# Kernel optimization log

Hardware: AMD Instinct MI355X
Metric: run time of the kernel (lower is better)

Reference implementation:

```python
import jax, jax.numpy as jnp
import numpy as np

N_NODES = 4096
D_FEAT = 256


def _interp_linear_2x(x):
    # Matches F.interpolate(mode='linear', scale_factor=2, align_corners=False)
    # applied along the node axis. x: [N, D] -> [2N, D]
    n = x.shape[0]
    out_i = jnp.arange(2 * n, dtype=jnp.float32)
    src = jnp.clip((out_i + 0.5) * 0.5 - 0.5, 0.0, float(n - 1))
    i0 = jnp.floor(src).astype(jnp.int32)
    i1 = jnp.minimum(i0 + 1, n - 1)
    w = (src - i0.astype(jnp.float32))[:, None]
    return x[i0] * (1.0 - w) + x[i1] * w


def _nearest_neighbor_idx(x):
    # argmin over pairwise Euclidean distances with diagonal excluded.
    # Squared distances give the same argmin as torch.cdist.
    sq = jnp.sum(x * x, axis=1)
    d2 = sq[:, None] + sq[None, :] - 2.0 * (x @ x.T)  # [2N, 2N]
    m = x.shape[0]
    d2 = jnp.where(jnp.eye(m, dtype=bool), jnp.inf, d2)
    return jnp.argmin(d2, axis=1)


def setup_inputs() -> dict:
    key = jax.random.key(0)
    k1, k2, k3, k4 = jax.random.split(key, 4)
    x = jax.random.normal(k1, (N_NODES, D_FEAT), dtype=jnp.float32)
    adj = jax.random.uniform(k2, (N_NODES, N_NODES), dtype=jnp.float32)
    # Xavier-uniform-ish init for the two GCN weights
    lim = float(np.sqrt(6.0 / (D_FEAT + D_FEAT)))
    W1 = jax.random.uniform(k3, (D_FEAT, D_FEAT), jnp.float32, -lim, lim)
    W2 = jax.random.uniform(k4, (D_FEAT, D_FEAT), jnp.float32, -lim, lim)
    return {"x": x, "adj": adj, "W1": W1, "W2": W2}


def reference(x, adj, W1, W2):
    # conv1: adj @ (x @ W1)
    h = adj @ (x @ W1)                      # [N, D]
    x2 = _interp_linear_2x(h)               # [2N, D]
    # nearest-neighbor one-hot adjacency, then conv2.
    # one_hot(nn_idx) @ support == support[nn_idx] (exact same math)
    nn_idx = _nearest_neighbor_idx(x2)      # [2N]
    support = x2 @ W2                       # [2N, D]
    return support[nn_idx]                  # [2N, D]
```

## Files before the change

### kernel.cpp

```cpp
#include <hip/hip_runtime.h>
#include <hip/hip_bf16.h>
#include <cstdint>

typedef __attribute__((ext_vector_type(8))) __bf16 bf16x8;
typedef __attribute__((ext_vector_type(4))) float f32x4;

static __device__ __forceinline__ unsigned short f2bf(float f) {
  return __builtin_bit_cast(unsigned short, (__bf16)f);
}
static __device__ __forceinline__ unsigned pack2(float a, float b) {
  return (unsigned)f2bf(a) | ((unsigned)f2bf(b) << 16);
}
#define GLDS(src, dst) __builtin_amdgcn_global_load_lds( \
    (const __attribute__((address_space(1))) void*)(src), \
    (__attribute__((address_space(3))) void*)(dst), 16, 0, 0)


__global__ void transpose_w_kernel(const float* __restrict__ W1, const float* __restrict__ W2,
                                   unsigned short* __restrict__ W1t, unsigned short* __restrict__ W2t) {
  int i = blockIdx.x * 256 + threadIdx.x;
  int k = i >> 8, n = i & 255;
  W1t[n * 256 + k] = f2bf(W1[k * 256 + n]);
  W2t[n * 256 + k] = f2bf(W2[k * 256 + n]);
}

__global__ void upsample_kernel(const unsigned short* __restrict__ hs,
                                unsigned short* __restrict__ x2b, float* __restrict__ sq) {
  int row = blockIdx.x * 4 + (threadIdx.x >> 6);
  int c = (threadIdx.x & 63) * 4;
  float s = (row + 0.5f) * 0.5f - 0.5f;
  s = fminf(fmaxf(s, 0.0f), 4095.0f);
  float fl = floorf(s);
  int i0 = (int)fl;
  int i1 = min((int)fl + 1, 4095);
  float w = s - fl;
  float v0[4] = {0.f, 0.f, 0.f, 0.f}, v1[4] = {0.f, 0.f, 0.f, 0.f};
  #pragma unroll
  for (int k = 0; k < 8; ++k) {
    ushort4 u0 = *(const ushort4*)&hs[(size_t)k * 4096 * 256 + i0 * 256 + c];
    ushort4 u1 = *(const ushort4*)&hs[(size_t)k * 4096 * 256 + i1 * 256 + c];
    v0[0] += __builtin_bit_cast(float, (unsigned)u0.x << 16);
    v0[1] += __builtin_bit_cast(float, (unsigned)u0.y << 16);
    v0[2] += __builtin_bit_cast(float, (unsigned)u0.z << 16);
    v0[3] += __builtin_bit_cast(float, (unsigned)u0.w << 16);
    v1[0] += __builtin_bit_cast(float, (unsigned)u1.x << 16);
    v1[1] += __builtin_bit_cast(float, (unsigned)u1.y << 16);
    v1[2] += __builtin_bit_cast(float, (unsigned)u1.z << 16);
    v1[3] += __builtin_bit_cast(float, (unsigned)u1.w << 16);
  }
  float p = 0.f;
  ushort4 st;
  unsigned short* sp = (unsigned short*)&st;
  #pragma unroll
  for (int e = 0; e < 4; ++e) {
    float v = v0[e] * (1.0f - w) + v1[e] * w;
    sp[e] = f2bf(v);
    p += v * v;
  }
  *(ushort4*)&x2b[(size_t)row * 256 + c] = st;
  #pragma unroll
  for (int m = 32; m > 0; m >>= 1) p += __shfl_down(p, m, 64);
  if ((threadIdx.x & 63) == 0) sq[row] = p;
}

__global__ void argmin_reduce_kernel(const unsigned* __restrict__ pv,
                                     unsigned* __restrict__ pck) {
  int row = blockIdx.x * 256 + threadIdx.x;
  int cr = row >> 7;
  unsigned best = 0xFFFFFFFFu;
  for (int c = 0; c <= cr; ++c) best = min(best, pv[(size_t)c * 8192 + row]);
  for (int c = cr + 1; c < 64; ++c) best = min(best, pv[(size_t)(64 + c) * 8192 + row]);
  pck[row] = best & 0x1FFFu;
}

__global__ void gather_kernel(const float* __restrict__ support,
                              const unsigned* __restrict__ pck,
                              float* __restrict__ out) {
  int gid = blockIdx.x * 256 + threadIdx.x;
  int row = gid >> 6;
  int c4 = (gid & 63) * 4;
  unsigned idx = pck[row];
  *(float4*)&out[(size_t)row * 256 + c4] = *(const float4*)&support[(size_t)idx * 256 + c4];
}

__launch_bounds__(256, 3)
__global__ void gram_kernel(const unsigned short* __restrict__ X,
                            const float* __restrict__ sq,
                            unsigned* __restrict__ pv) {
  __shared__ alignas(16) unsigned short As[128 * 64];
  __shared__ alignas(16) unsigned short Bs[128 * 64];
  __shared__ unsigned mrgr[2][128];
  __shared__ unsigned mrgc[2][128];

  const int tid = threadIdx.x;
  const int wid = tid >> 6;
  const int lane = tid & 63;
  const int g = lane >> 4, lr = lane & 15;
  const int wr = wid >> 1, wc = wid & 1;

  int t = blockIdx.x;
  int bi = (int)((sqrtf(8.0f * (float)t + 1.0f) - 1.0f) * 0.5f);
  while ((bi + 1) * (bi + 2) / 2 <= t) ++bi;
  while (bi * (bi + 1) / 2 > t) --bi;
  const int bx = bi;
  const int by = t - bi * (bi + 1) / 2;
  const int m0 = bx * 128;
  const int n0 = by * 128;
  const bool diag = (bx == by);

  const int srow = tid >> 3;
  const int ssc = (tid & 7) ^ (srow & 7);
  const unsigned short* aBase = X + (size_t)(m0 + srow) * 256 + ssc * 8;
  const unsigned short* bBase = X + (size_t)(n0 + srow) * 256 + ssc * 8;
  unsigned short* const aDst = As + (size_t)(tid >> 6) * 512;
  unsigned short* const bDst = Bs + (size_t)(tid >> 6) * 512;

  f32x4 acc[4][4];
  const f32x4 fzero = {0.f, 0.f, 0.f, 0.f};
  #pragma unroll
  for (int i = 0; i < 4; ++i)
    #pragma unroll
    for (int j = 0; j < 4; ++j) acc[i][j] = fzero;

  #pragma unroll
  for (int ks = 0; ks < 4; ++ks) {
    #pragma unroll
    for (int it = 0; it < 4; ++it)
      GLDS(aBase + it * 8192 + ks * 64, aDst + it * 2048);
    #pragma unroll
    for (int it = 0; it < 4; ++it)
      GLDS(bBase + it * 8192 + ks * 64, bDst + it * 2048);
    __syncthreads();
    #pragma unroll
    for (int kk = 0; kk < 2; ++kk) {
      const int ch = (kk * 4 + g) ^ (lr & 7);
      bf16x8 b[4];
      #pragma unroll
      for (int j = 0; j < 4; ++j)
        b[j] = *(const bf16x8*)&Bs[(wc * 64 + j * 16 + lr) * 64 + ch * 8];
      #pragma unroll
      for (int i = 0; i < 4; ++i) {
        bf16x8 a = *(const bf16x8*)&As[(wr * 64 + i * 16 + lr) * 64 + ch * 8];
        #pragma unroll
        for (int j = 0; j < 4; ++j)
          acc[i][j] = __builtin_amdgcn_mfma_f32_16x16x32_bf16(a, b[j], acc[i][j], 0, 0, 0);
      }
    }
    __syncthreads();
  }

  int jcol[4];
  float sqj[4];
  unsigned ckey[4];
  #pragma unroll
  for (int j = 0; j < 4; ++j) {
    jcol[j] = n0 + wc * 64 + j * 16 + lr;
    sqj[j] = sq[jcol[j]];
    ckey[j] = 0xFFFFFFFFu;
  }
  #pragma unroll
  for (int i = 0; i < 4; ++i) {
    #pragma unroll
    for (int r = 0; r < 4; ++r) {
      const int lrow = wr * 64 + i * 16 + g * 4 + r;
      const int irow = m0 + lrow;
      const float sqi = sq[irow];
      unsigned rk = 0xFFFFFFFFu;
      #pragma unroll
      for (int j = 0; j < 4; ++j) {
        float v = fmaf(-2.0f, acc[i][j][r], sqi + sqj[j]);
        unsigned bits = __float_as_uint(v) & 0xFFFFE000u;
        unsigned krow = bits | (unsigned)jcol[j];
        if (diag && jcol[j] == irow) krow = 0xFFFFFFFFu;
        rk = min(rk, krow);
        if (!diag) ckey[j] = min(ckey[j], bits | (unsigned)irow);
      }
      #pragma unroll
      for (int m = 1; m < 16; m <<= 1)
        rk = min(rk, (unsigned)__shfl_xor((int)rk, m, 64));
      if (lr == 0) mrgr[wc][lrow] = rk;
    }
  }
  if (!diag) {
    #pragma unroll
    for (int j = 0; j < 4; ++j) {
      ckey[j] = min(ckey[j], (unsigned)__shfl_xor((int)ckey[j], 16, 64));
      ckey[j] = min(ckey[j], (unsigned)__shfl_xor((int)ckey[j], 32, 64));
      if (g == 0) mrgc[wr][wc * 64 + j * 16 + lr] = ckey[j];
    }
  }
  __syncthreads();
  if (tid < 128) {
    pv[(size_t)by * 8192 + m0 + tid] = min(mrgr[0][tid], mrgr[1][tid]);
  } else if (!diag) {
    int c = tid - 128;
    pv[(size_t)(64 + bx) * 8192 + n0 + c] = min(mrgc[0][c], mrgc[1][c]);
  }
}

template <int BM, int BN, int WAVES_M, int KT, int EPI, bool AF32>
__launch_bounds__(256)
__global__ void gemm_nt_kernel(const void* __restrict__ Ap, int lda,
                               const unsigned short* __restrict__ Bp, int ldb,
                               int M, int N,
                               float* __restrict__ Cf,
                               unsigned short* __restrict__ Cb) {
  constexpr int BK = 64;
  constexpr int NT = KT / BK;
  constexpr int WAVES_N = 4 / WAVES_M;
  constexpr int WM = BM / WAVES_M;
  constexpr int WN = BN / WAVES_N;
  constexpr int FM = WM / 16;
  constexpr int FN = WN / 16;
  constexpr int ASLOT = BM * 8;
  constexpr int AITER = (ASLOT + 255) / 256;
  constexpr int BITER = (BN * 8) / 256;

  __shared__ alignas(16) unsigned short As[BM * BK];
  __shared__ alignas(16) unsigned short Bs[BN * BK];

  const int tid = threadIdx.x;
  const int wid = tid >> 6;
  const int lane = tid & 63;
  const int g = lane >> 4;
  const int lr = lane & 15;
  const int wr = wid / WAVES_N;
  const int wc = wid % WAVES_N;
  const int m0 = blockIdx.x * BM;
  const int n0 = (EPI == 3) ? 0 : blockIdx.y * BN;
  const int kbase = (EPI == 3) ? blockIdx.y * KT : 0;
  if constexpr (EPI == 3) Cb += (size_t)blockIdx.y * (size_t)M * (size_t)N;

  const int srow = tid >> 3;
  const int ssc = (tid & 7) ^ (srow & 7);
  const float* aBaseF = (const float*)Ap + (size_t)(m0 + srow) * (size_t)lda + kbase + ssc * 8;
  const unsigned short* aBaseH = (const unsigned short*)Ap + (size_t)(m0 + srow) * (size_t)lda + kbase + ssc * 8;
  const unsigned short* bBase = Bp + (size_t)(n0 + srow) * (size_t)ldb + kbase + ssc * 8;
  unsigned short* const sDst = As + (size_t)wid * 512;
  unsigned short* const bDst = Bs + (size_t)wid * 512;

  f32x4 acc[FM][FN];
  const f32x4 fzero = {0.f, 0.f, 0.f, 0.f};
  #pragma unroll
  for (int i = 0; i < FM; ++i)
    #pragma unroll
    for (int j = 0; j < FN; ++j) acc[i][j] = fzero;

  #pragma unroll
  for (int t = 0; t < NT; ++t) {
    #pragma unroll
    for (int it = 0; it < BITER; ++it)
      GLDS(bBase + (size_t)it * 32 * ldb + t * 64, bDst + it * 2048);
    if constexpr (AF32) {
      #pragma unroll
      for (int it = 0; it < AITER; ++it) {
        if (ASLOT % 256 == 0 || it * 256 + tid < ASLOT) {
          const float* src = aBaseF + (size_t)it * 32 * lda + t * 64;
          float4 f0 = *(const float4*)src;
          float4 f1 = *(const float4*)(src + 4);
          uint4 pk = { pack2(f0.x, f0.y), pack2(f0.z, f0.w),
                       pack2(f1.x, f1.y), pack2(f1.z, f1.w) };
          *(uint4*)&As[(it * 32 + srow) * BK + (tid & 7) * 8] = pk;
        }
      }
    } else {
      #pragma unroll
      for (int it = 0; it < AITER; ++it)
        GLDS(aBaseH + (size_t)it * 32 * lda + t * 64, sDst + it * 2048);
    }
    __syncthreads();
    #pragma unroll
    for (int kk = 0; kk < 2; ++kk) {
      const int ch = (kk * 4 + g) ^ (lr & 7);
      bf16x8 a[FM], b[FN];
      #pragma unroll
      for (int i = 0; i < FM; ++i)
        a[i] = *(const bf16x8*)&As[(wr * WM + i * 16 + lr) * BK + ch * 8];
      #pragma unroll
      for (int j = 0; j < FN; ++j)
        b[j] = *(const bf16x8*)&Bs[(wc * WN + j * 16 + lr) * BK + ch * 8];
      #pragma unroll
      for (int i = 0; i < FM; ++i)
        #pragma unroll
        for (int j = 0; j < FN; ++j)
          acc[i][j] = __builtin_amdgcn_mfma_f32_16x16x32_bf16(a[i], b[j], acc[i][j], 0, 0, 0);
    }
    __syncthreads();
  }

  const int rowb = wr * WM;
  const int colb = wc * WN;
  if constexpr (EPI == 0) {
    #pragma unroll
    for (int i = 0; i < FM; ++i) {
      int mrow = m0 + rowb + i * 16 + g * 4;
      #pragma unroll
      for (int j = 0; j < FN; ++j) {
        int col = n0 + colb + j * 16 + lr;
        #pragma unroll
        for (int r = 0; r < 4; ++r)
          Cf[(size_t)(mrow + r) * N + col] = acc[i][j][r];
      }
    }
  } else if constexpr (EPI == 1) {
    #pragma unroll
    for (int i = 0; i < FM; ++i) {
      int mrow = m0 + rowb + i * 16 + g * 4;
      #pragma unroll
      for (int j = 0; j < FN; ++j) {
        int col = n0 + colb + j * 16 + lr;
        ushort4 st;
        st.x = f2bf(acc[i][j][0]);
        st.y = f2bf(acc[i][j][1]);
        st.z = f2bf(acc[i][j][2]);
        st.w = f2bf(acc[i][j][3]);
        *(ushort4*)&Cb[(size_t)col * M + mrow] = st;
      }
    }
  } else {
    #pragma unroll
    for (int i = 0; i < FM; ++i) {
      int mrow = m0 + rowb + i * 16 + g * 4;
      #pragma unroll
      for (int j = 0; j < FN; ++j) {
        int col = n0 + colb + j * 16 + lr;
        #pragma unroll
        for (int r = 0; r < 4; ++r)
          Cb[(size_t)(mrow + r) * N + col] = f2bf(acc[i][j][r]);
      }
    }
  }
}


extern "C" void kernel_launch(void* const* d_in, const int* in_sizes, int n_in,
                              void* d_out, int out_size, void* d_ws, size_t ws_size,
                              hipStream_t stream) {
  (void)in_sizes; (void)n_in; (void)out_size; (void)ws_size;
  const float* x   = (const float*)d_in[0];
  const float* adj = (const float*)d_in[1];
  const float* W1  = (const float*)d_in[2];
  const float* W2  = (const float*)d_in[3];
  float* out = (float*)d_out;

  char* p = (char*)d_ws;
  unsigned short* Tt  = (unsigned short*)p;  p += 4096 * 256 * 2;
  char* R             = p;                   p += 16 * 1024 * 1024;
  unsigned short* x2b = (unsigned short*)p;  p += 8192 * 256 * 2;
  float* sqv          = (float*)p;           p += 8192 * 4;
  unsigned* pck       = (unsigned*)p;        p += 8192 * 4;
  unsigned short* W1t = (unsigned short*)p;  p += 256 * 256 * 2;
  unsigned short* W2t = (unsigned short*)p;  p += 256 * 256 * 2;

  unsigned short* hs = (unsigned short*)R;
  unsigned* pv       = (unsigned*)R;
  float* support     = (float*)R;

  transpose_w_kernel<<<256, 256, 0, stream>>>(W1, W2, W1t, W2t);

  gemm_nt_kernel<64, 64, 4, 256, 1, true><<<dim3(64, 4), 256, 0, stream>>>(
      x, 256, W1t, 256, 4096, 256, nullptr, Tt);

  gemm_nt_kernel<64, 256, 1, 512, 3, true><<<dim3(64, 8), 256, 0, stream>>>(
      adj, 4096, Tt, 4096, 4096, 256, nullptr, hs);

  upsample_kernel<<<2048, 256, 0, stream>>>(hs, x2b, sqv);

  gram_kernel<<<2080, 256, 0, stream>>>(x2b, sqv, pv);

  argmin_reduce_kernel<<<32, 256, 0, stream>>>(pv, pck);

  gemm_nt_kernel<64, 64, 4, 256, 0, false><<<dim3(128, 4), 256, 0, stream>>>(
      x2b, 256, W2t, 256, 8192, 256, support, nullptr);

  gather_kernel<<<2048, 256, 0, stream>>>(support, pck, out);
}
```

Before: 102.4 us.

## Fuse nearest-neighbor gather into W2 GEMM and skip B-tile load on diagonal gram tiles

The final GEMM now gathers its A rows by nearest-neighbor index, so it computes x2[nn]@W2 and writes straight to the output. This removes the intermediate support buffer and the separate gather kernel launch. Separately, diagonal gram tiles reuse the A tile in shared memory as B instead of loading the same data twice. The gathered rows make A-loads non-contiguous, and rounding now happens at a different point but is mathematically equivalent.

```diff
diff --git a/kernel.cpp b/kernel.cpp
--- a/kernel.cpp
+++ b/kernel.cpp
@@ -73,16 +73,6 @@
   pck[row] = best & 0x1FFFu;
 }
 
-__global__ void gather_kernel(const float* __restrict__ support,
-                              const unsigned* __restrict__ pck,
-                              float* __restrict__ out) {
-  int gid = blockIdx.x * 256 + threadIdx.x;
-  int row = gid >> 6;
-  int c4 = (gid & 63) * 4;
-  unsigned idx = pck[row];
-  *(float4*)&out[(size_t)row * 256 + c4] = *(const float4*)&support[(size_t)idx * 256 + c4];
-}
-
 __launch_bounds__(256, 3)
 __global__ void gram_kernel(const unsigned short* __restrict__ X,
                             const float* __restrict__ sq,
@@ -114,6 +104,7 @@
   const unsigned short* bBase = X + (size_t)(n0 + srow) * 256 + ssc * 8;
   unsigned short* const aDst = As + (size_t)(tid >> 6) * 512;
   unsigned short* const bDst = Bs + (size_t)(tid >> 6) * 512;
+  const unsigned short* const Bsrc = diag ? As : Bs;
 
   f32x4 acc[4][4];
   const f32x4 fzero = {0.f, 0.f, 0.f, 0.f};
@@ -127,9 +118,11 @@
     #pragma unroll
     for (int it = 0; it < 4; ++it)
       GLDS(aBase + it * 8192 + ks * 64, aDst + it * 2048);
-    #pragma unroll
-    for (int it = 0; it < 4; ++it)
-      GLDS(bBase + it * 8192 + ks * 64, bDst + it * 2048);
+    if (!diag) {
+      #pragma unroll
+      for (int it = 0; it < 4; ++it)
+        GLDS(bBase + it * 8192 + ks * 64, bDst + it * 2048);
+    }
     __syncthreads();
     #pragma unroll
     for (int kk = 0; kk < 2; ++kk) {
@@ -137,7 +130,7 @@
       bf16x8 b[4];
       #pragma unroll
       for (int j = 0; j < 4; ++j)
-        b[j] = *(const bf16x8*)&Bs[(wc * 64 + j * 16 + lr) * 64 + ch * 8];
+        b[j] = *(const bf16x8*)&Bsrc[(wc * 64 + j * 16 + lr) * 64 + ch * 8];
       #pragma unroll
       for (int i = 0; i < 4; ++i) {
         bf16x8 a = *(const bf16x8*)&As[(wr * 64 + i * 16 + lr) * 64 + ch * 8];
@@ -198,13 +191,14 @@
   }
 }
 
-template <int BM, int BN, int WAVES_M, int KT, int EPI, bool AF32>
+template <int BM, int BN, int WAVES_M, int KT, int EPI, bool AF32, bool GATHER>
 __launch_bounds__(256)
 __global__ void gemm_nt_kernel(const void* __restrict__ Ap, int lda,
                                const unsigned short* __restrict__ Bp, int ldb,
                                int M, int N,
                                float* __restrict__ Cf,
-                               unsigned short* __restrict__ Cb) {
+                               unsigned short* __restrict__ Cb,
+                               const unsigned* __restrict__ gidx) {
   constexpr int BK = 64;
   constexpr int NT = KT / BK;
   constexpr int WAVES_N = 4 / WAVES_M;
@@ -233,8 +227,18 @@
 
   const int srow = tid >> 3;
   const int ssc = (tid & 7) ^ (srow & 7);
-  const float* aBaseF = (const float*)Ap + (size_t)(m0 + srow) * (size_t)lda + kbase + ssc * 8;
-  const unsigned short* aBaseH = (const unsigned short*)Ap + (size_t)(m0 + srow) * (size_t)lda + kbase + ssc * 8;
+  const float* aBF[AITER];
+  const unsigned short* aBH[AITER];
+  #pragma unroll
+  for (int it = 0; it < AITER; ++it) {
+    int r = m0 + srow + it * 32;
+    if constexpr (AF32) {
+      aBF[it] = (const float*)Ap + (size_t)r * (size_t)lda + kbase + ssc * 8;
+    } else {
+      int sr = GATHER ? (int)gidx[r] : r;
+      aBH[it] = (const unsigned short*)Ap + (size_t)sr * (size_t)lda + kbase + ssc * 8;
+    }
+  }
   const unsigned short* bBase = Bp + (size_t)(n0 + srow) * (size_t)ldb + kbase + ssc * 8;
   unsigned short* const sDst = As + (size_t)wid * 512;
   unsigned short* const bDst = Bs + (size_t)wid * 512;
@@ -255,7 +259,7 @@
       #pragma unroll
       for (int it = 0; it < AITER; ++it) {
         if (ASLOT % 256 == 0 || it * 256 + tid < ASLOT) {
-          const float* src = aBaseF + (size_t)it * 32 * lda + t * 64;
+          const float* src = aBF[it] + t * 64;
           float4 f0 = *(const float4*)src;
           float4 f1 = *(const float4*)(src + 4);
           uint4 pk = { pack2(f0.x, f0.y), pack2(f0.z, f0.w),
@@ -266,7 +270,7 @@
     } else {
       #pragma unroll
       for (int it = 0; it < AITER; ++it)
-        GLDS(aBaseH + (size_t)it * 32 * lda + t * 64, sDst + it * 2048);
+        GLDS(aBH[it] + t * 64, sDst + it * 2048);
     }
     __syncthreads();
     #pragma unroll
@@ -354,15 +358,14 @@
 
   unsigned short* hs = (unsigned short*)R;
   unsigned* pv       = (unsigned*)R;
-  float* support     = (float*)R;
 
   transpose_w_kernel<<<256, 256, 0, stream>>>(W1, W2, W1t, W2t);
 
-  gemm_nt_kernel<64, 64, 4, 256, 1, true><<<dim3(64, 4), 256, 0, stream>>>(
-      x, 256, W1t, 256, 4096, 256, nullptr, Tt);
-
-  gemm_nt_kernel<64, 256, 1, 512, 3, true><<<dim3(64, 8), 256, 0, stream>>>(
-      adj, 4096, Tt, 4096, 4096, 256, nullptr, hs);
+  gemm_nt_kernel<64, 64, 4, 256, 1, true, false><<<dim3(64, 4), 256, 0, stream>>>(
+      x, 256, W1t, 256, 4096, 256, nullptr, Tt, nullptr);
+
+  gemm_nt_kernel<64, 256, 1, 512, 3, true, false><<<dim3(64, 8), 256, 0, stream>>>(
+      adj, 4096, Tt, 4096, 4096, 256, nullptr, hs, nullptr);
 
   upsample_kernel<<<2048, 256, 0, stream>>>(hs, x2b, sqv);
 
@@ -370,8 +373,6 @@
 
   argmin_reduce_kernel<<<32, 256, 0, stream>>>(pv, pck);
 
-  gemm_nt_kernel<64, 64, 4, 256, 0, false><<<dim3(128, 4), 256, 0, stream>>>(
-      x2b, 256, W2t, 256, 8192, 256, support, nullptr);
-
-  gather_kernel<<<2048, 256, 0, stream>>>(support, pck, out);
-}
+  gemm_nt_kernel<64, 64, 4, 256, 0, false, true><<<dim3(128, 4), 256, 0, stream>>>(
+      x2b, 256, W2t, 256, 8192, 256, out, nullptr, pck);
+}
```

Result: faster. 98.03 us (-4.2%).
